# Performance work log

Hardware: AMD Instinct MI355X
Metric: run time of the kernel (lower is better)

Reference implementation:

```python
import jax, jax.numpy as jnp
import numpy as np

N, E, D, L = 40000, 640000, 128, 4

def setup_inputs() -> dict:
    key = jax.random.key(0)
    ks = jax.random.split(key, 4)
    x = jax.random.normal(ks[0], (N, D), dtype=jnp.float32)
    edge_index = jax.random.randint(ks[1], (2, E), 0, N)
    edge_weight = jax.random.uniform(ks[2], (E,), dtype=jnp.float32)
    W = jax.random.normal(ks[3], (L, D, D), dtype=jnp.float32) / np.float32(np.sqrt(D))
    b = jnp.zeros((L, D), jnp.float32)
    gamma = jnp.ones((L, D), jnp.float32)
    beta = jnp.zeros((L, D), jnp.float32)
    return dict(x=x, edge_index=edge_index, edge_weight=edge_weight, W=W, b=b, gamma=gamma, beta=beta)

def _gcn_norm(edge_index, edge_weight, n):
    # PyG gcn_norm: add self loops (weight 1), symmetric D^-1/2 A D^-1/2
    loops = jnp.arange(n)
    src = jnp.concatenate([edge_index[0], loops])
    dst = jnp.concatenate([edge_index[1], loops])
    ew = jnp.concatenate([edge_weight, jnp.ones((n,), edge_weight.dtype)])
    deg = jax.ops.segment_sum(ew, dst, num_segments=n)
    dis = jnp.where(deg > 0, jax.lax.rsqrt(jnp.maximum(deg, 1e-12)), 0.0)
    return src, dst, dis[src] * ew * dis[dst]

def _batchnorm(h, g, bta):
    # training-mode BatchNorm1d over the node axis, biased variance, eps=1e-5
    mu = h.mean(0)
    var = h.var(0)
    return g * (h - mu) * jax.lax.rsqrt(var + 1e-5) + bta

def reference(x, edge_index, edge_weight, W, b, gamma, beta):
    n = x.shape[0]
    n_layers = W.shape[0]
    src, dst, norm = _gcn_norm(edge_index, edge_weight, n)
    x0 = x  # decoded_reshaped_x for skip connections
    for i in range(n_layers):
        h = x @ W[i]                                   # [N, D] linear (GCNConv.lin)
        msg = h[src] * norm[:, None]                   # gather + scale, [E+N, D]
        h = jax.ops.segment_sum(msg, dst, num_segments=n) + b[i]
        if i < n_layers - 1:
            h = jax.nn.relu(h)
        h = h + x0                                     # skip connection
        if i != n_layers - 2:
            h = _batchnorm(h, gamma[i], beta[i])
        x = h
    return x
```

## Files before the change

kernel.cpp:

```cpp
#include <hip/hip_runtime.h>
#include <cstdint>
#include <cstddef>

constexpr int N = 40000;
constexpr int E = 640000;
constexpr int D = 128;
constexpr int NBKT = 157;
constexpr int BCAP = 5120;
constexpr int AGG_GRID = 2500;

typedef _Float16 half8 __attribute__((ext_vector_type(8)));
typedef float f32x4 __attribute__((ext_vector_type(4)));
typedef unsigned long long ull;

__device__ __forceinline__ unsigned int pack_rec(int idx, float v) {
  union { _Float16 h; unsigned short us; } c; c.h = (_Float16)v;
  return (unsigned int)idx | ((unsigned int)c.us << 16);
}


__global__ void k_zero(uint4* __restrict__ p) {
  int i = blockIdx.x * 256 + threadIdx.x;
  if (i < 2136) p[i] = make_uint4(0u, 0u, 0u, 0u);
}


__global__ void k_bigprep(const int* __restrict__ ei, const float* __restrict__ ew,
                          const float* __restrict__ X, _Float16* __restrict__ Xh,
                          const float* __restrict__ W, _Float16* __restrict__ Wt,
                          ull* __restrict__ binned, int* __restrict__ bktcnt) {
  int bid = blockIdx.x, t = threadIdx.x;
  if (bid < NBKT) {
    __shared__ int lhist[NBKT], lbase[NBKT], lrank[NBKT];
    if (t < NBKT) { lhist[t] = 0; lrank[t] = 0; }
    __syncthreads();
    int e16 = bid * 256 + t;
    bool act = (e16 < E / 16);
    int4 s4[4], d4[4]; float4 w4[4];
    if (act) {
#pragma unroll
      for (int u = 0; u < 4; ++u) {
        s4[u] = ((const int4*)ei)[e16 * 4 + u];
        d4[u] = ((const int4*)(ei + E))[e16 * 4 + u];
        w4[u] = ((const float4*)ew)[e16 * 4 + u];
      }
#pragma unroll
      for (int u = 0; u < 4; ++u) {
        atomicAdd(&lhist[d4[u].x >> 8], 1); atomicAdd(&lhist[d4[u].y >> 8], 1);
        atomicAdd(&lhist[d4[u].z >> 8], 1); atomicAdd(&lhist[d4[u].w >> 8], 1);
      }
    }
    __syncthreads();
    if (t < NBKT && lhist[t] > 0) lbase[t] = atomicAdd(&bktcnt[t], lhist[t]);
    __syncthreads();
    if (act) {
      auto emit = [&](int s, int dcol, float w) {
        int bkt = dcol >> 8;
        int rank = atomicAdd(&lrank[bkt], 1);
        int pos = lbase[bkt] + rank;
        ull rec = (ull)(unsigned)(s & 0xFFFF)
                | ((ull)(unsigned)(dcol & 255) << 16)
                | ((ull)__float2uint_rn(w * 67108864.0f) << 24);
        if (pos < BCAP) binned[(size_t)bkt * BCAP + pos] = rec;
      };
#pragma unroll
      for (int u = 0; u < 4; ++u) {
        emit(s4[u].x, d4[u].x, w4[u].x); emit(s4[u].y, d4[u].y, w4[u].y);
        emit(s4[u].z, d4[u].z, w4[u].z); emit(s4[u].w, d4[u].w, w4[u].w);
      }
    }
  } else if (bid < 2657) {
    int i = (bid - NBKT) * 256 + t;
    float4 v0 = ((const float4*)X)[i * 2];
    float4 v1 = ((const float4*)X)[i * 2 + 1];
    half8 h;
    h[0] = (_Float16)v0.x; h[1] = (_Float16)v0.y; h[2] = (_Float16)v0.z; h[3] = (_Float16)v0.w;
    h[4] = (_Float16)v1.x; h[5] = (_Float16)v1.y; h[6] = (_Float16)v1.z; h[7] = (_Float16)v1.w;
    ((half8*)Xh)[i] = h;
  } else {
    int o = (bid - 2657) * 256 + t;
    int l = o >> 14, rem = o & 16383, c = rem >> 7, k = rem & 127;
    Wt[o] = (_Float16)W[l * 16384 + k * 128 + c];
  }
}


__global__ __launch_bounds__(256) void k_bstats(const ull* __restrict__ binned,
    const int* __restrict__ bktcnt, float* __restrict__ dis, int* __restrict__ rowc,
    int* __restrict__ bsum, int* __restrict__ hist) {
  __shared__ ull acc[256];
  __shared__ int lhist[64];
  __shared__ int red[256];
  int bkt = blockIdx.x, t = threadIdx.x;
  acc[t] = 0ULL;
  if (t < 64) lhist[t] = 0;
  __syncthreads();
  int cnt = min(bktcnt[bkt], BCAP);
  const ull* bp = binned + (size_t)bkt * BCAP;
  for (int e = t; e < cnt; e += 256) {
    ull r = bp[e];
    int local = (int)((r >> 16) & 255);
    atomicAdd(&acc[local], (1ULL << 40) | (r >> 24));
  }
  __syncthreads();
  int row = bkt * 256 + t;
  int c = 0;
  if (row < N) {
    ull a = acc[t];
    c = (int)(a >> 40) + 1;
    float deg = (float)(a & ((1ULL << 40) - 1)) * (1.0f / 67108864.0f);
    dis[row] = rsqrtf(deg + 1.0f);
    rowc[row] = c;
    atomicAdd(&lhist[min(c, 63)], 1);
  }
  red[t] = c;
  __syncthreads();
  for (int off = 128; off > 0; off >>= 1) {
    if (t < off) red[t] += red[t + off];
    __syncthreads();
  }
  if (t == 0) bsum[bkt] = red[0];
  if (t < 64 && lhist[t] > 0) atomicAdd(&hist[t], lhist[t]);
}

__global__ void k_scan_bsums(const int* __restrict__ bsum, int* __restrict__ bpre) {
  __shared__ int s[256];
  int t = threadIdx.x;
  s[t] = (t < NBKT) ? bsum[t] : 0;
  __syncthreads();
  for (int off = 1; off < 256; off <<= 1) {
    int v = s[t];
    int add = (t >= off) ? s[t - off] : 0;
    __syncthreads();
    s[t] = v + add;
    __syncthreads();
  }
  if (t < NBKT) bpre[t] = (t == 0) ? 0 : s[t - 1];
}


__global__ void k_histscan(const int* __restrict__ hist, int* __restrict__ histstart,
                           int* __restrict__ histcur) {
  int b = threadIdx.x;
  int s = 0;
  for (int b2 = b + 1; b2 < 64; ++b2) s += hist[b2];
  histstart[b] = s;
  histcur[b] = s;
}


__device__ __forceinline__ void gemm_body(int bid, int tid, const _Float16* __restrict__ X,
    const _Float16* __restrict__ Wt, const float* __restrict__ sums,
    const float* __restrict__ gamma, const float* __restrict__ beta, int useBN,
    const float* __restrict__ dis, _Float16* __restrict__ Hout,
    float* scl, float* shf) {
  if (tid < 128) {
    if (useBN) {
      float s = 0.f, s2 = 0.f;
#pragma unroll
      for (int r = 0; r < 8; ++r) { s += sums[r * 256 + tid]; s2 += sums[r * 256 + 128 + tid]; }
      float mu = s * (1.0f / N);
      float var = s2 * (1.0f / N) - mu * mu;
      float rs = rsqrtf(var + 1e-5f);
      float sc = gamma[tid] * rs;
      scl[tid] = sc;
      shf[tid] = beta[tid] - mu * sc;
    } else {
      scl[tid] = 1.0f;
      shf[tid] = 0.0f;
    }
  }
  __syncthreads();

  int wv = tid >> 6, lane = tid & 63;
  int fr = lane & 15, kg = lane >> 4;
  int arow = bid * 64 + wv * 16 + fr;
  const _Float16* xrow = X + (size_t)arow * D;

  half8 af[4];
#pragma unroll
  for (int kc = 0; kc < 4; ++kc) {
    int k0 = kc * 32 + kg * 8;
    half8 xr = *(const half8*)&xrow[k0];
    half8 a;
#pragma unroll
    for (int u = 0; u < 8; ++u)
      a[u] = (_Float16)fmaf((float)xr[u], scl[k0 + u], shf[k0 + u]);
    af[kc] = a;
  }

  f32x4 acc[8];
#pragma unroll
  for (int ct = 0; ct < 8; ++ct) acc[ct] = (f32x4){0.f, 0.f, 0.f, 0.f};

#pragma unroll
  for (int ct = 0; ct < 8; ++ct) {
    const _Float16* wcol = Wt + (size_t)(ct * 16 + fr) * 128;
#pragma unroll
    for (int kc = 0; kc < 4; ++kc) {
      half8 bf = *(const half8*)&wcol[kc * 32 + kg * 8];
      acc[ct] = __builtin_amdgcn_mfma_f32_16x16x32_f16(af[kc], bf, acc[ct], 0, 0, 0);
    }
  }

  int orow0 = bid * 64 + wv * 16 + kg * 4;
#pragma unroll
  for (int rg = 0; rg < 4; ++rg) {
    int grow = orow0 + rg;
    float dsv = dis[grow];
    _Float16* hrow = Hout + (size_t)grow * D;
#pragma unroll
    for (int ct = 0; ct < 8; ++ct)
      hrow[ct * 16 + fr] = (_Float16)(acc[ct][rg] * dsv);
  }
}

__global__ __launch_bounds__(256) void k_gemm(const _Float16* __restrict__ X,
    const _Float16* __restrict__ Wt, const float* __restrict__ sums,
    const float* __restrict__ gamma, const float* __restrict__ beta, int useBN,
    const float* __restrict__ dis, _Float16* __restrict__ Hout) {
  __shared__ float scl[128], shf[128];
  gemm_body(blockIdx.x, threadIdx.x, X, Wt, sums, gamma, beta, useBN, dis, Hout, scl, shf);
}


__global__ __launch_bounds__(256) void k_gemm0_fill(const _Float16* __restrict__ X,
    const _Float16* __restrict__ Wt, const float* __restrict__ dis,
    _Float16* __restrict__ Hout,
    const int* __restrict__ rowc, const int* __restrict__ bpre,
    const ull* __restrict__ binned, const int* __restrict__ bktcnt,
    unsigned int* __restrict__ cv, int* __restrict__ offs,
    int* __restrict__ histcur, int* __restrict__ perm) {
  int bid = blockIdx.x, t = threadIdx.x;
  if (bid < 625) {
    __shared__ float scl[128], shf[128];
    gemm_body(bid, t, X, Wt, (const float*)nullptr, (const float*)nullptr,
              (const float*)nullptr, 0, dis, Hout, scl, shf);
  } else if (bid < 625 + NBKT) {
    int bkt = bid - 625;
    __shared__ int lcur[256];
    __shared__ int s[256];
    int row = bkt * 256 + t;
    int c = (row < N) ? rowc[row] : 0;
    s[t] = c;
    __syncthreads();
    for (int off = 1; off < 256; off <<= 1) {
      int v = s[t];
      int add = (t >= off) ? s[t - off] : 0;
      __syncthreads();
      s[t] = v + add;
      __syncthreads();
    }
    int run = bpre[bkt] + s[t] - c;
    if (row < N) {
      offs[row] = run;
      cv[run] = pack_rec(row, 1.0f);
      lcur[t] = run + 1;
    } else {
      lcur[t] = 0;
    }
    if (row == N - 1) offs[N] = N + E;
    __syncthreads();
    int cnt = min(bktcnt[bkt], BCAP);
    const ull* bp = binned + (size_t)bkt * BCAP;
    for (int e = t; e < cnt; e += 256) {
      ull r = bp[e];
      int local = (int)((r >> 16) & 255);
      int srcv = (int)(r & 0xFFFFu);
      float w = (float)(unsigned)(r >> 24) * (1.0f / 67108864.0f);
      int slot = atomicAdd(&lcur[local], 1);
      cv[slot] = pack_rec(srcv, w);
    }
  } else {
    __shared__ int lhist[64], lbase[64];
    if (t < 64) lhist[t] = 0;
    __syncthreads();
    int i = (bid - (625 + NBKT)) * 256 + t;
    bool valid = (i < N);
    int bin = 0, myrank = 0;
    if (valid) {
      int c = rowc[i];
      bin = min(c, 63);
      myrank = atomicAdd(&lhist[bin], 1);
    }
    __syncthreads();
    if (t < 64 && lhist[t] > 0) lbase[t] = atomicAdd(&histcur[t], lhist[t]);
    __syncthreads();
    if (valid) perm[lbase[bin] + myrank] = i;
  }
}


__global__ __launch_bounds__(256) void k_agg(const uint4* __restrict__ Hu4,
    const int* __restrict__ offs, const unsigned int* __restrict__ cv,
    const float* __restrict__ dis, const float* __restrict__ bias,
    const uint4* __restrict__ x0h, const int* __restrict__ perm,
    int doRelu, int doStats, int outF32,
    _Float16* __restrict__ Hout16, float* __restrict__ Houtf, float* __restrict__ sums) {
  int t = threadIdx.x;
  int sl = t & 15;
  int g = t >> 4;
  int row = perm[blockIdx.x * 16 + g];
  float4 bv0 = ((const float4*)bias)[sl * 2];
  float4 bv1 = ((const float4*)bias)[sl * 2 + 1];

  int e0 = offs[row], e1 = offs[row + 1];
  float a[8];
#pragma unroll
  for (int k = 0; k < 8; ++k) a[k] = 0.f;
  for (int eb = e0; eb < e1; eb += 16) {
    int m = min(16, e1 - eb);
    unsigned int rec = 0;
    if (sl < m) rec = cv[eb + sl];
#pragma unroll 8
    for (int j = 0; j < m; ++j) {
      unsigned int rj = __shfl(rec, j, 16);
      int sj = (int)(rj & 0xFFFFu);
      union { unsigned short us; _Float16 h; } vh; vh.us = (unsigned short)(rj >> 16);
      float vj = (float)vh.h;
      union { uint4 u; _Float16 hh[8]; } cu;
      cu.u = Hu4[(size_t)sj * 16 + sl];
#pragma unroll
      for (int k = 0; k < 8; ++k) a[k] = fmaf((float)cu.hh[k], vj, a[k]);
    }
  }
  float dr = dis[row];
  union { uint4 u; _Float16 hh[8]; } xc;
  xc.u = x0h[(size_t)row * 16 + sl];
  float rr[8];
  rr[0] = fmaf(a[0], dr, bv0.x); rr[1] = fmaf(a[1], dr, bv0.y);
  rr[2] = fmaf(a[2], dr, bv0.z); rr[3] = fmaf(a[3], dr, bv0.w);
  rr[4] = fmaf(a[4], dr, bv1.x); rr[5] = fmaf(a[5], dr, bv1.y);
  rr[6] = fmaf(a[6], dr, bv1.z); rr[7] = fmaf(a[7], dr, bv1.w);
  if (doRelu) {
#pragma unroll
    for (int k = 0; k < 8; ++k) rr[k] = fmaxf(rr[k], 0.f);
  }
#pragma unroll
  for (int k = 0; k < 8; ++k) rr[k] += (float)xc.hh[k];
  if (outF32) {
    float4 o0, o1;
    o0.x = rr[0]; o0.y = rr[1]; o0.z = rr[2]; o0.w = rr[3];
    o1.x = rr[4]; o1.y = rr[5]; o1.z = rr[6]; o1.w = rr[7];
    ((float4*)Houtf)[(size_t)row * 32 + sl * 2] = o0;
    ((float4*)Houtf)[(size_t)row * 32 + sl * 2 + 1] = o1;
  } else {
    union { uint4 u; _Float16 hh[8]; } ov;
#pragma unroll
    for (int k = 0; k < 8; ++k) ov.hh[k] = (_Float16)rr[k];
    ((uint4*)Hout16)[(size_t)row * 16 + sl] = ov.u;
  }

  if (doStats) {
    __shared__ float reds[16 * 128], reds2[16 * 128];
#pragma unroll
    for (int k = 0; k < 8; ++k) {
      reds[g * 128 + sl * 8 + k] = rr[k];
      reds2[g * 128 + sl * 8 + k] = rr[k] * rr[k];
    }
    __syncthreads();
    if (t < 128) {
      float ts = 0.f, ts2 = 0.f;
#pragma unroll
      for (int j = 0; j < 16; ++j) { ts += reds[j * 128 + t]; ts2 += reds2[j * 128 + t]; }
      int rep = blockIdx.x & 7;
      atomicAdd(&sums[rep * 256 + t], ts);
      atomicAdd(&sums[rep * 256 + 128 + t], ts2);
    }
  }
}


__global__ __launch_bounds__(256) void k_bnapply(float* __restrict__ H,
    const float* __restrict__ sums, const float* __restrict__ gamma,
    const float* __restrict__ beta) {
  __shared__ float scl[128], shf[128];
  int t = threadIdx.x;
  if (t < 128) {
    float s = 0.f, s2 = 0.f;
#pragma unroll
    for (int r = 0; r < 8; ++r) { s += sums[r * 256 + t]; s2 += sums[r * 256 + 128 + t]; }
    float mu = s * (1.0f / N);
    float var = s2 * (1.0f / N) - mu * mu;
    float rs = rsqrtf(var + 1e-5f);
    float sc = gamma[t] * rs;
    scl[t] = sc;
    shf[t] = beta[t] - mu * sc;
  }
  __syncthreads();
  size_t i = (size_t)blockIdx.x * 256 + t;
  float4 v = ((const float4*)H)[i];
  int c = (int)(i & 31) * 4;
  v.x = fmaf(v.x, scl[c + 0], shf[c + 0]);
  v.y = fmaf(v.y, scl[c + 1], shf[c + 1]);
  v.z = fmaf(v.z, scl[c + 2], shf[c + 2]);
  v.w = fmaf(v.w, scl[c + 3], shf[c + 3]);
  ((float4*)H)[i] = v;
}


extern "C" void kernel_launch(void* const* d_in, const int* in_sizes, int n_in,
                              void* d_out, int out_size, void* d_ws, size_t ws_size,
                              hipStream_t stream) {
  const float* x     = (const float*)d_in[0];
  const int*   ei    = (const int*)d_in[1];
  const float* ew    = (const float*)d_in[2];
  const float* W     = (const float*)d_in[3];
  const float* b     = (const float*)d_in[4];
  const float* gamma = (const float*)d_in[5];
  const float* beta  = (const float*)d_in[6];
  float* out = (float*)d_out;

  char* ws = (char*)d_ws;
  _Float16* hlin   = (_Float16*)ws;
  _Float16* hagg16 = (_Float16*)(ws + 10240000);
  _Float16* xh     = (_Float16*)(ws + 20480000);
  float* sums4    = (float*)(ws + 30720000);
  int*   hist     = (int*)  (ws + 30752768);
  int*   histstart= (int*)  (ws + 30753024);
  int*   histcur  = (int*)  (ws + 30753280);
  int*   bktcnt   = (int*)  (ws + 30753536);
  float* dis      = (float*)(ws + 30754176);
  int*   offs     = (int*)  (ws + 30914176);
  int*   rowc     = (int*)  (ws + 31074192);
  unsigned int* cv= (unsigned int*)(ws + 31234192);
  int*   perm     = (int*)  (ws + 33954192);
  int*   bsum     = (int*)  (ws + 34114192);
  int*   bpre     = (int*)  (ws + 34114832);
  _Float16* Wt    = (_Float16*)(ws + 34115472);
  ull* binned     = (ull*)  (ws + 34246544);

  k_zero<<<9, 256, 0, stream>>>((uint4*)sums4);
  k_bigprep<<<2913, 256, 0, stream>>>(ei, ew, x, xh, W, Wt, binned, bktcnt);
  k_bstats<<<NBKT, 256, 0, stream>>>(binned, bktcnt, dis, rowc, bsum, hist);
  k_scan_bsums<<<1, 256, 0, stream>>>(bsum, bpre);
  k_histscan<<<1, 64, 0, stream>>>(hist, histstart, histcur);

  for (int l = 0; l < 4; ++l) {
    const _Float16* xin = (l == 0) ? xh : hagg16;
    if (l == 0) {
      k_gemm0_fill<<<625 + NBKT + 157, 256, 0, stream>>>(xin, Wt, dis, hlin,
                                                         rowc, bpre, binned, bktcnt,
                                                         cv, offs, histcur, perm);
    } else {
      int useBN = (l == 1 || l == 2) ? 1 : 0;
      const float* sprev = sums4 + (size_t)(l - 1) * 2048;
      k_gemm<<<N / 64, 256, 0, stream>>>(xin, Wt + (size_t)l * 16384, sprev,
                                         gamma + (size_t)(l - 1) * D,
                                         beta + (size_t)(l - 1) * D, useBN, dis, hlin);
    }
    int doStats = (l != 2) ? 1 : 0;
    int doRelu = (l < 3) ? 1 : 0;
    int outF32 = (l == 3) ? 1 : 0;
    k_agg<<<AGG_GRID, 256, 0, stream>>>((const uint4*)hlin, offs, cv, dis,
                                        b + (size_t)l * D, (const uint4*)xh, perm,
                                        doRelu, doStats, outF32, hagg16, out,
                                        sums4 + (size_t)l * 2048);
  }
  k_bnapply<<<(N * D / 4) / 256, 256, 0, stream>>>(out, sums4 + 3 * 2048,
                                                   gamma + 3 * D, beta + 3 * D);
}
```

Measured before the change: 232.7 us.

## Fold scan kernels into bstats via last-block pattern; batch agg gathers

After: 230.5 us. Within noise of the previous version (-0.9%).

```diff
diff --git a/kernel.cpp b/kernel.cpp
--- a/kernel.cpp
+++ b/kernel.cpp
@@ -87,10 +87,12 @@
 
 __global__ __launch_bounds__(256) void k_bstats(const ull* __restrict__ binned,
     const int* __restrict__ bktcnt, float* __restrict__ dis, int* __restrict__ rowc,
-    int* __restrict__ bsum, int* __restrict__ hist) {
+    int* __restrict__ bsum, int* __restrict__ hist, int* __restrict__ bpre,
+    int* __restrict__ histcur, unsigned int* __restrict__ done) {
   __shared__ ull acc[256];
   __shared__ int lhist[64];
   __shared__ int red[256];
+  __shared__ int amlast;
   int bkt = blockIdx.x, t = threadIdx.x;
   acc[t] = 0ULL;
   if (t < 64) lhist[t] = 0;
@@ -121,31 +123,29 @@
   }
   if (t == 0) bsum[bkt] = red[0];
   if (t < 64 && lhist[t] > 0) atomicAdd(&hist[t], lhist[t]);
-}
-
-__global__ void k_scan_bsums(const int* __restrict__ bsum, int* __restrict__ bpre) {
-  __shared__ int s[256];
-  int t = threadIdx.x;
-  s[t] = (t < NBKT) ? bsum[t] : 0;
+  __syncthreads();
+  if (t == 0) {
+    __threadfence();
+    amlast = (atomicAdd(done, 1u) == NBKT - 1);
+  }
+  __syncthreads();
+  if (!amlast) return;
+  __threadfence();
+  red[t] = (t < NBKT) ? bsum[t] : 0;
   __syncthreads();
   for (int off = 1; off < 256; off <<= 1) {
-    int v = s[t];
-    int add = (t >= off) ? s[t - off] : 0;
-    __syncthreads();
-    s[t] = v + add;
-    __syncthreads();
-  }
-  if (t < NBKT) bpre[t] = (t == 0) ? 0 : s[t - 1];
-}
-
-
-__global__ void k_histscan(const int* __restrict__ hist, int* __restrict__ histstart,
-                           int* __restrict__ histcur) {
-  int b = threadIdx.x;
-  int s = 0;
-  for (int b2 = b + 1; b2 < 64; ++b2) s += hist[b2];
-  histstart[b] = s;
-  histcur[b] = s;
+    int v = red[t];
+    int add = (t >= off) ? red[t - off] : 0;
+    __syncthreads();
+    red[t] = v + add;
+    __syncthreads();
+  }
+  if (t < NBKT) bpre[t] = (t == 0) ? 0 : red[t - 1];
+  if (t < 64) {
+    int s = 0;
+    for (int b2 = t + 1; b2 < 64; ++b2) s += hist[b2];
+    histcur[t] = s;
+  }
 }
 
 
@@ -303,6 +303,7 @@
   int row = perm[blockIdx.x * 16 + g];
   float4 bv0 = ((const float4*)bias)[sl * 2];
   float4 bv1 = ((const float4*)bias)[sl * 2 + 1];
+  const uint4* hp = Hu4 + sl;
 
   int e0 = offs[row], e1 = offs[row + 1];
   float a[8];
@@ -312,16 +313,26 @@
     int m = min(16, e1 - eb);
     unsigned int rec = 0;
     if (sl < m) rec = cv[eb + sl];
-#pragma unroll 8
-    for (int j = 0; j < m; ++j) {
-      unsigned int rj = __shfl(rec, j, 16);
-      int sj = (int)(rj & 0xFFFFu);
-      union { unsigned short us; _Float16 h; } vh; vh.us = (unsigned short)(rj >> 16);
-      float vj = (float)vh.h;
-      union { uint4 u; _Float16 hh[8]; } cu;
-      cu.u = Hu4[(size_t)sj * 16 + sl];
-#pragma unroll
-      for (int k = 0; k < 8; ++k) a[k] = fmaf((float)cu.hh[k], vj, a[k]);
+#pragma unroll 1
+    for (int g8 = 0; g8 < 2; ++g8) {
+      int b0 = g8 * 8;
+      if (b0 >= m) break;
+      uint4 cu[8]; float vv[8];
+#pragma unroll
+      for (int j = 0; j < 8; ++j) {
+        int jj = b0 + j;
+        int jc = (jj < m) ? jj : (m - 1);
+        unsigned int rj = __shfl(rec, jc, 16);
+        union { unsigned short us; _Float16 h; } vh; vh.us = (unsigned short)(rj >> 16);
+        vv[j] = (jj < m) ? (float)vh.h : 0.f;
+        cu[j] = hp[(size_t)(rj & 0xFFFFu) * 16];
+      }
+#pragma unroll
+      for (int j = 0; j < 8; ++j) {
+        union { uint4 u; _Float16 hh[8]; } c8; c8.u = cu[j];
+#pragma unroll
+        for (int k = 0; k < 8; ++k) a[k] = fmaf((float)c8.hh[k], vv[j], a[k]);
+      }
     }
   }
   float dr = dis[row];
@@ -417,9 +428,9 @@
   _Float16* xh     = (_Float16*)(ws + 20480000);
   float* sums4    = (float*)(ws + 30720000);
   int*   hist     = (int*)  (ws + 30752768);
-  int*   histstart= (int*)  (ws + 30753024);
-  int*   histcur  = (int*)  (ws + 30753280);
-  int*   bktcnt   = (int*)  (ws + 30753536);
+  int*   histcur  = (int*)  (ws + 30753024);
+  int*   bktcnt   = (int*)  (ws + 30753280);
+  unsigned int* done = (unsigned int*)(ws + 30753920);
   float* dis      = (float*)(ws + 30754176);
   int*   offs     = (int*)  (ws + 30914176);
   int*   rowc     = (int*)  (ws + 31074192);
@@ -432,9 +443,8 @@
 
   k_zero<<<9, 256, 0, stream>>>((uint4*)sums4);
   k_bigprep<<<2913, 256, 0, stream>>>(ei, ew, x, xh, W, Wt, binned, bktcnt);
-  k_bstats<<<NBKT, 256, 0, stream>>>(binned, bktcnt, dis, rowc, bsum, hist);
-  k_scan_bsums<<<1, 256, 0, stream>>>(bsum, bpre);
-  k_histscan<<<1, 64, 0, stream>>>(hist, histstart, histcur);
+  k_bstats<<<NBKT, 256, 0, stream>>>(binned, bktcnt, dis, rowc, bsum, hist,
+                                     bpre, histcur, done);
 
   for (int l = 0; l < 4; ++l) {
     const _Float16* xin = (l == 0) ? xh : hagg16;
```
